# Optimization experiments

Measured on AMD Instinct MI355X. Metric: run time of the kernel, lower is better.

## Reference

```python
import jax, jax.numpy as jnp
import numpy as np

B, H, W, C = 4, 224, 224, 256
HEADS = 8
WIN = 7
N = WIN * WIN  # 49 tokens per window
MLP_HID = 4 * C
EPS = 1e-5


def _rel_index(w):
    coords = np.stack(np.meshgrid(np.arange(w), np.arange(w), indexing='ij'))  # (2,w,w)
    cf = coords.reshape(2, -1)                       # (2, w*w)
    rc = cf[:, :, None] - cf[:, None, :]             # (2, N, N)
    rc = rc.transpose(1, 2, 0).astype(np.int64)      # (N, N, 2)
    rc[:, :, 0] += w - 1
    rc[:, :, 1] += w - 1
    rc[:, :, 0] *= 2 * w - 1
    return jnp.asarray(rc.sum(-1), dtype=jnp.int32)  # (N, N)


def setup_inputs() -> dict:
    key = jax.random.key(0)
    ks = jax.random.split(key, 6)
    std = 0.02
    return {
        'x': jax.random.normal(ks[0], (B, H, W, C), dtype=jnp.float32),
        'norm1_g': jnp.ones((C,), jnp.float32),
        'norm1_b': jnp.zeros((C,), jnp.float32),
        'qkv_w': jax.random.normal(ks[1], (3 * C, C), jnp.float32) * std,
        'qkv_b': jnp.zeros((3 * C,), jnp.float32),
        'bias_table': jax.random.normal(ks[2], ((2 * WIN - 1) ** 2, HEADS), jnp.float32) * std,
        'proj_w': jax.random.normal(ks[3], (C, C), jnp.float32) * std,
        'proj_b': jnp.zeros((C,), jnp.float32),
        'norm2_g': jnp.ones((C,), jnp.float32),
        'norm2_b': jnp.zeros((C,), jnp.float32),
        'fc1_w': jax.random.normal(ks[4], (MLP_HID, C), jnp.float32) * std,
        'fc1_b': jnp.zeros((MLP_HID,), jnp.float32),
        'fc2_w': jax.random.normal(ks[5], (C, MLP_HID), jnp.float32) * std,
        'fc2_b': jnp.zeros((C,), jnp.float32),
        'rel_index': _rel_index(WIN),
    }


def _layernorm(x, g, b):
    mu = jnp.mean(x, axis=-1, keepdims=True)
    var = jnp.mean(jnp.square(x - mu), axis=-1, keepdims=True)
    return (x - mu) * jax.lax.rsqrt(var + EPS) * g + b


def reference(x, norm1_g, norm1_b, qkv_w, qkv_b, bias_table, proj_w, proj_b,
              norm2_g, norm2_b, fc1_w, fc1_b, fc2_w, fc2_b, rel_index):
    Bc, Hc, Wc, Cc = x.shape
    d = Cc // HEADS
    scale = d ** -0.5
    nh, nw = Hc // WIN, Wc // WIN

    shortcut = x
    h = _layernorm(x, norm1_g, norm1_b)

    # window_partition: (B,H,W,C) -> (B*nW, N, C)
    wins = h.reshape(Bc, nh, WIN, nw, WIN, Cc).transpose(0, 1, 3, 2, 4, 5)
    wins = wins.reshape(-1, N, Cc)

    # qkv projection and split into heads
    qkv = wins @ qkv_w.T + qkv_b                                  # (Bw, N, 3C)
    qkv = qkv.reshape(-1, N, 3, HEADS, d).transpose(2, 0, 3, 1, 4)  # (3, Bw, h, N, d)
    q, k, v = qkv[0], qkv[1], qkv[2]

    attn = jnp.einsum('bhnd,bhmd->bhnm', q, k) * scale            # (Bw, h, N, N)
    bias = bias_table[rel_index.reshape(-1)].reshape(N, N, HEADS).transpose(2, 0, 1)
    attn = jax.nn.softmax(attn + bias[None], axis=-1)

    o = jnp.einsum('bhnm,bhmd->bhnd', attn, v)                    # (Bw, h, N, d)
    o = o.transpose(0, 2, 1, 3).reshape(-1, N, Cc)
    o = o @ proj_w.T + proj_b

    # window_reverse: (B*nW, N, C) -> (B,H,W,C)
    o = o.reshape(Bc, nh, nw, WIN, WIN, Cc).transpose(0, 1, 3, 2, 4, 5)
    o = o.reshape(Bc, Hc, Wc, Cc)

    x = shortcut + o
    h2 = _layernorm(x, norm2_g, norm2_b)
    m = jax.nn.gelu(h2 @ fc1_w.T + fc1_b, approximate=False) @ fc2_w.T + fc2_b
    return x + m
```

## Files before the change

kernel.cpp:

```cpp
#include <hip/hip_runtime.h>

typedef unsigned short u16;
typedef __bf16 bf16x8 __attribute__((ext_vector_type(8)));
typedef float f32x4 __attribute__((ext_vector_type(4)));

#define TOKENS 200704
#define QK_ELEMS 51380224UL

__device__ __forceinline__ u16 f2b(float f) {
    __bf16 h = (__bf16)f;
    return __builtin_bit_cast(u16, h);
}

#define GLDS(g, l) __builtin_amdgcn_global_load_lds( \
    (const __attribute__((address_space(1))) void*)(g), \
    (__attribute__((address_space(3))) void*)(l), 16, 0, 0)

#define MFMA __builtin_amdgcn_mfma_f32_16x16x32_bf16

template<int EPI, int WR, int WC>
__global__ __launch_bounds__(512, 4)
void gemm_t(const u16* __restrict__ A, const u16* __restrict__ W,
            const float* __restrict__ bias, int nt, int K,
            u16* __restrict__ outb, float* __restrict__ outf,
            const float* __restrict__ res,
            const float* __restrict__ g2, const float* __restrict__ b2,
            u16* __restrict__ h2o)
{
    constexpr int BM = WR * 64, BN = WC * 64;
    constexpr int ACH = BM / 16;
    constexpr int TCH = (BM + BN) / 16;
    __shared__ u16 As[3][BM * 32];
    __shared__ u16 Bs[3][BN * 32];
    __shared__ float red[EPI == 1 ? 2 * 128 * 4 : 1];

    const int tid  = threadIdx.x;
    const int wave = tid >> 6, lane = tid & 63;

    const int nwg = gridDim.x, bidO = blockIdx.x;
    const int qq = nwg >> 3, rr = nwg & 7;
    const int xcd = bidO & 7, idxx = bidO >> 3;
    const int bid = (xcd < rr) ? (xcd * (qq + 1) + idxx)
                               : (rr * (qq + 1) + (xcd - rr) * qq + idxx);

    const int bm = bid / nt, bn = bid % nt;
    const long m0 = (long)bm * BM;
    const int  n0 = bn * BN;
    const int wr = wave / WC, wc = wave % WC;
    const int lr = lane & 15, lg = lane >> 4;
    const int ccol_s = (((lane & 3) ^ ((lane >> 3) & 3)) * 8);
    const int swzr = (lg ^ ((lr >> 1) & 3)) * 8;

    f32x4 acc[4][4] = {};

    auto stage = [&](int buf, int k0) {
#pragma unroll
        for (int p = 0; p < TCH / 8; ++p) {
            const int q = p * 8 + wave;
            const int rq = (q < ACH) ? q : q - ACH;
            const int row = rq * 16 + (lane >> 2);
            if (q < ACH)
                GLDS(A + (m0 + row) * (long)K + k0 + ccol_s, &As[buf][rq * 512]);
            else
                GLDS(W + (long)(n0 + row) * K + k0 + ccol_s, &Bs[buf][rq * 512]);
        }
    };

    auto compute = [&](int buf) {
        bf16x8 af[4], bfr[4];
#pragma unroll
        for (int fm = 0; fm < 4; ++fm)
            af[fm] = *reinterpret_cast<const bf16x8*>(
                &As[buf][(wr * 64 + fm * 16 + lr) * 32 + swzr]);
#pragma unroll
        for (int fn = 0; fn < 4; ++fn)
            bfr[fn] = *reinterpret_cast<const bf16x8*>(
                &Bs[buf][(wc * 64 + fn * 16 + lr) * 32 + swzr]);
        __builtin_amdgcn_s_setprio(1);
#pragma unroll
        for (int fm = 0; fm < 4; ++fm)
#pragma unroll
            for (int fn = 0; fn < 4; ++fn)
                acc[fm][fn] = MFMA(af[fm], bfr[fn], acc[fm][fn], 0, 0, 0);
        __builtin_amdgcn_s_setprio(0);
    };

    const int nk = K >> 5;
    stage(0, 0);
    stage(1, 32);
    stage(2, 64);
    int k = 96;
    int buf = 0;
    for (int t = 0; t < nk; ++t) {
        if (t + 2 < nk)      asm volatile("s_waitcnt vmcnt(6)" ::: "memory");
        else if (t + 1 < nk) asm volatile("s_waitcnt vmcnt(3)" ::: "memory");
        else                 asm volatile("s_waitcnt vmcnt(0)" ::: "memory");
        __builtin_amdgcn_s_barrier();
        __builtin_amdgcn_sched_barrier(0);
        compute(buf);
        __builtin_amdgcn_s_barrier();
        __builtin_amdgcn_sched_barrier(0);
        if (t + 3 < nk) {
            stage(buf, k); k += 32;
            __builtin_amdgcn_sched_barrier(0);
        }
        buf = (buf == 2) ? 0 : buf + 1;
    }

    if constexpr (EPI == 0 || EPI == 2) {
        u16* st = &As[0][0];
        float bb4[4], sc4[4];
#pragma unroll
        for (int fn = 0; fn < 4; ++fn) {
            const int n = n0 + wc * 64 + fn * 16 + lr;
            bb4[fn] = bias[n];
            sc4[fn] = (EPI == 0 && (n >> 8) == 0) ? 0.17677669529663687f : 1.0f;
        }
        const size_t secbase = (EPI == 0)
            ? (size_t)(n0 >> 8) * QK_ELEMS + (size_t)(n0 & 255) : 0;
#pragma unroll
        for (int h = 0; h < 2; ++h) {
            if ((wr >> 1) == h) {
#pragma unroll
                for (int fm = 0; fm < 4; ++fm) {
#pragma unroll
                    for (int r = 0; r < 4; ++r) {
                        const int lrow = (wr & 1) * 64 + fm * 16 + lg * 4 + r;
                        const int swb = ((lrow >> 2) & 3) << 1;
#pragma unroll
                        for (int fn = 0; fn < 4; ++fn) {
                            const int col = wc * 64 + fn * 16 + lr;
                            const int cs = (col >> 3) ^ swb;
                            float v = acc[fm][fn][r] + bb4[fn];
                            u16 w;
                            if (EPI == 0) {
                                w = f2b(v * sc4[fn]);
                            } else {
                                const float s = v * (1.5957691216f + 0.07135481627f * v * v);
                                w = f2b(v * __builtin_amdgcn_rcpf(1.0f + __expf(-s)));
                            }
                            st[lrow * 128 + cs * 8 + (col & 7)] = w;
                        }
                    }
                }
            }
            asm volatile("s_waitcnt lgkmcnt(0)" ::: "memory");
            __builtin_amdgcn_s_barrier();
#pragma unroll
            for (int it = 0; it < 4; ++it) {
                const int u = it * 512 + tid;
                const int row = u >> 4, chunk = u & 15;
                const int cs = chunk ^ (((row >> 2) & 3) << 1);
                const bf16x8 val = *reinterpret_cast<const bf16x8*>(st + row * 128 + cs * 8);
                const long m = m0 + h * 128 + row;
                if (EPI == 0) {
                    *reinterpret_cast<bf16x8*>(outb + secbase + m * 256 + (chunk << 3)) = val;
                } else {
                    *reinterpret_cast<bf16x8*>(outb + m * 1024 + n0 + (chunk << 3)) = val;
                }
            }
            if (h == 0) {
                asm volatile("s_waitcnt lgkmcnt(0)" ::: "memory");
                __builtin_amdgcn_s_barrier();
            }
        }
    } else if constexpr (EPI == 1) {
        float g2c[4], b2c[4];
#pragma unroll
        for (int fn = 0; fn < 4; ++fn) {
            const int n = wc * 64 + fn * 16 + lr;
            g2c[fn] = g2[n]; b2c[fn] = b2[n];
        }
#pragma unroll
        for (int fm = 0; fm < 4; ++fm) {
#pragma unroll
            for (int r = 0; r < 4; ++r) {
                const long m = m0 + wr * 64 + fm * 16 + lg * 4 + r;
                float s = 0.f, s2 = 0.f;
#pragma unroll
                for (int fn = 0; fn < 4; ++fn) {
                    const int n = wc * 64 + fn * 16 + lr;
                    const float x2 = acc[fm][fn][r] + bias[n] + res[m * 256 + n];
                    acc[fm][fn][r] = x2;
                    outf[m * 256 + n] = x2;
                    s += x2; s2 += x2 * x2;
                }
#pragma unroll
                for (int d = 1; d < 16; d <<= 1) { s += __shfl_xor(s, d); s2 += __shfl_xor(s2, d); }
                if (lr == 0) {
                    const int tok = wr * 64 + fm * 16 + lg * 4 + r;
                    red[(0 * 128 + tok) * 4 + wc] = s;
                    red[(1 * 128 + tok) * 4 + wc] = s2;
                }
            }
        }
        __syncthreads();
#pragma unroll
        for (int fm = 0; fm < 4; ++fm) {
#pragma unroll
            for (int r = 0; r < 4; ++r) {
                const int tok = wr * 64 + fm * 16 + lg * 4 + r;
                const float s = red[(0 * 128 + tok) * 4 + 0] + red[(0 * 128 + tok) * 4 + 1]
                              + red[(0 * 128 + tok) * 4 + 2] + red[(0 * 128 + tok) * 4 + 3];
                const float q = red[(1 * 128 + tok) * 4 + 0] + red[(1 * 128 + tok) * 4 + 1]
                              + red[(1 * 128 + tok) * 4 + 2] + red[(1 * 128 + tok) * 4 + 3];
                const float mu = s * 0.00390625f;
                const float rs = rsqrtf(q * 0.00390625f - mu * mu + 1e-5f);
                const long m = m0 + tok;
#pragma unroll
                for (int fn = 0; fn < 4; ++fn) {
                    const int n = wc * 64 + fn * 16 + lr;
                    h2o[m * 256 + n] = f2b((acc[fm][fn][r] - mu) * rs * g2c[fn] + b2c[fn]);
                }
            }
        }
    } else {
#pragma unroll
        for (int fm = 0; fm < 4; ++fm) {
#pragma unroll
            for (int r = 0; r < 4; ++r) {
                const long m = m0 + wr * 64 + fm * 16 + lg * 4 + r;
#pragma unroll
                for (int fn = 0; fn < 4; ++fn) {
                    const int n = n0 + wc * 64 + fn * 16 + lr;
                    outf[m * 256 + n] += acc[fm][fn][r] + bias[n];
                }
            }
        }
    }
}

__global__ __launch_bounds__(256)
void layernorm_k(const float* __restrict__ in, const float* __restrict__ g,
                 const float* __restrict__ bb, u16* __restrict__ out)
{
    const int token = blockIdx.x * 4 + (threadIdx.x >> 6);
    const int lane = threadIdx.x & 63;
    const float4 v = *reinterpret_cast<const float4*>(in + (size_t)token * 256 + lane * 4);
    float s  = v.x + v.y + v.z + v.w;
    float s2 = v.x * v.x + v.y * v.y + v.z * v.z + v.w * v.w;
#pragma unroll
    for (int m = 1; m < 64; m <<= 1) { s += __shfl_xor(s, m); s2 += __shfl_xor(s2, m); }
    const float mu  = s * (1.0f / 256.0f);
    const float var = s2 * (1.0f / 256.0f) - mu * mu;
    const float rs  = rsqrtf(var + 1e-5f);
    const float4 gv = *reinterpret_cast<const float4*>(g + lane * 4);
    const float4 bv = *reinterpret_cast<const float4*>(bb + lane * 4);
    ushort4 o;
    o.x = f2b((v.x - mu) * rs * gv.x + bv.x);
    o.y = f2b((v.y - mu) * rs * gv.y + bv.y);
    o.z = f2b((v.z - mu) * rs * gv.z + bv.z);
    o.w = f2b((v.w - mu) * rs * gv.w + bv.w);
    const int b = token / 50176, rem = token % 50176;
    const int y = rem / 224, x = rem % 224;
    const int win = (b * 32 + y / 7) * 32 + x / 7;
    const int pos = (y % 7) * 7 + (x % 7);
    const size_t wrow = (size_t)win * 49 + pos;
    *reinterpret_cast<ushort4*>(out + wrow * 256 + lane * 4) = o;
}

__global__ __launch_bounds__(256)
void attn_win(const u16* __restrict__ qkv, const float* __restrict__ biasF,
              u16* __restrict__ outb)
{
    __shared__ u16 plds[4][64 * 72];
    __shared__ u16 vlds[4][2048];
    const int wave = threadIdx.x >> 6, lane = threadIdx.x & 63;
    const int pair = blockIdx.x * 4 + wave;
    const int head = pair & 7, win = pair >> 3;
    const int lr = lane & 15, lg = lane >> 4;

    const u16* Q  = qkv + (size_t)win * 12544 + head * 32;
    const u16* Kp = Q + QK_ELEMS;
    const u16* Vp = Q + 2 * QK_ELEMS;

    bf16x8 qf[4], kf[4];
#pragma unroll
    for (int f = 0; f < 4; ++f) {
        int n = f * 16 + lr; n = n > 48 ? 48 : n;
        qf[f] = *reinterpret_cast<const bf16x8*>(Q  + n * 256 + lg * 8);
        kf[f] = *reinterpret_cast<const bf16x8*>(Kp + n * 256 + lg * 8);
    }

    u16* vl = &vlds[wave][0];
    {
        const int posh = lane >> 1, dsub = (lane & 1) * 8;
#pragma unroll
        for (int db = 0; db < 2; ++db)
#pragma unroll
            for (int half = 0; half < 2; ++half) {
                int pos = half * 32 + posh; if (pos > 48) pos = 48;
                GLDS(Vp + pos * 256 + db * 16 + dsub, vl + db * 1024 + half * 512);
            }
    }

    f32x4 s[4][4] = {};
#pragma unroll
    for (int fm = 0; fm < 4; ++fm)
#pragma unroll
        for (int fn = 0; fn < 4; ++fn)
            s[fm][fn] = MFMA(qf[fm], kf[fn], s[fm][fn], 0, 0, 0);

    const float* bfh = biasF + head * 4096;
    u16* pl = &plds[wave][0];
#pragma unroll
    for (int fm = 0; fm < 4; ++fm) {
        f32x4 bb[4];
#pragma unroll
        for (int fn = 0; fn < 4; ++fn)
            bb[fn] = *reinterpret_cast<const f32x4*>(bfh + ((fm * 4 + fn) << 8) + (lane << 2));
#pragma unroll
        for (int r = 0; r < 4; ++r) {
            const int row = fm * 16 + lg * 4 + r;
            float v0 = s[fm][0][r] + bb[0][r];
            float v1 = s[fm][1][r] + bb[1][r];
            float v2 = s[fm][2][r] + bb[2][r];
            float v3 = s[fm][3][r] + bb[3][r];
            float mx = fmaxf(fmaxf(v0, v1), fmaxf(v2, v3));
#pragma unroll
            for (int d = 1; d < 16; d <<= 1) mx = fmaxf(mx, __shfl_xor(mx, d));
            const float p0 = __expf(v0 - mx), p1 = __expf(v1 - mx);
            const float p2 = __expf(v2 - mx), p3 = __expf(v3 - mx);
            float sum = p0 + p1 + p2 + p3;
#pragma unroll
            for (int d = 1; d < 16; d <<= 1) sum += __shfl_xor(sum, d);
            const float rinv = __builtin_amdgcn_rcpf(sum);
            pl[row * 72 +  0 + lr] = f2b(p0 * rinv);
            pl[row * 72 + 16 + lr] = f2b(p1 * rinv);
            pl[row * 72 + 32 + lr] = f2b(p2 * rinv);
            pl[row * 72 + 48 + lr] = f2b(p3 * rinv);
        }
    }

    asm volatile("s_waitcnt vmcnt(0)" ::: "memory");
    if (lane < 60) {
        const int db = lane / 30, ix = lane % 30;
        f32x4 z = {0.f, 0.f, 0.f, 0.f};
        *reinterpret_cast<f32x4*>(vl + db * 1024 + 784 + ix * 8) = z;
    }
    asm volatile("s_waitcnt lgkmcnt(0)" ::: "memory");
    __builtin_amdgcn_sched_barrier(0);

    const unsigned VB = (unsigned)(unsigned long)
        (__attribute__((address_space(3))) u16*)vl;
    unsigned long long trv[2][2][2];
#pragma unroll
    for (int kc = 0; kc < 2; ++kc)
#pragma unroll
        for (int f2 = 0; f2 < 2; ++f2) {
            const unsigned va = VB + f2 * 2048 + kc * 1024 + lg * 256 + lr * 2;
            asm volatile("ds_read_b64_tr_b16 %0, %1"
                         : "=v"(trv[kc][f2][0]) : "v"(va));
            asm volatile("ds_read_b64_tr_b16 %0, %1 offset:128"
                         : "=v"(trv[kc][f2][1]) : "v"(va));
        }
    asm volatile("s_waitcnt lgkmcnt(0)" ::: "memory");
    __builtin_amdgcn_sched_barrier(0);

    f32x4 o[4][2] = {};
#pragma unroll
    for (int kc = 0; kc < 2; ++kc) {
#pragma unroll
        for (int fm = 0; fm < 4; ++fm) {
            const bf16x8 pa = *reinterpret_cast<const bf16x8*>(
                pl + (fm * 16 + lr) * 72 + kc * 32 + lg * 8);
#pragma unroll
            for (int f2 = 0; f2 < 2; ++f2) {
                union { unsigned long long q[2]; bf16x8 v; } u;
                u.q[0] = trv[kc][f2][0]; u.q[1] = trv[kc][f2][1];
                o[fm][f2] = MFMA(pa, u.v, o[fm][f2], 0, 0, 0);
            }
        }
    }

    const int b = win >> 10, rem = win & 1023, wy = rem >> 5, wx = rem & 31;
#pragma unroll
    for (int fm = 0; fm < 4; ++fm) {
#pragma unroll
        for (int r = 0; r < 4; ++r) {
            const int tok = fm * 16 + lg * 4 + r;
            if (tok > 48) continue;
            const int y = wy * 7 + tok / 7, xx = wx * 7 + tok % 7;
            const size_t mrow = ((size_t)(b * 224 + y)) * 224 + xx;
#pragma unroll
            for (int f2 = 0; f2 < 2; ++f2)
                outb[mrow * 256 + head * 32 + f2 * 16 + lr] = f2b(o[fm][f2][r]);
        }
    }
}

__global__ __launch_bounds__(256)
void cvt_w(const float* __restrict__ qw, const float* __restrict__ pw,
           const float* __restrict__ f1, const float* __restrict__ f2,
           u16* __restrict__ outw)
{
    const int t = blockIdx.x * 256 + threadIdx.x;
    float v;
    if (t < 196608) v = qw[t];
    else if (t < 262144) v = pw[t - 196608];
    else if (t < 524288) v = f1[t - 262144];
    else v = f2[t - 524288];
    outw[t] = f2b(v);
}

__global__ __launch_bounds__(256)
void bias_pre(const float* __restrict__ btab, const int* __restrict__ relidx,
              float* __restrict__ biasF)
{
    const int t = blockIdx.x * 256 + threadIdx.x;
    const int head = t >> 10, rem = t & 1023;
    const int fr = rem >> 6, lane = rem & 63;
    const int fm = fr >> 2, fn = fr & 3;
    const int lr = lane & 15, lg = lane >> 4;
    const int col = fn * 16 + lr;
    f32x4 o;
#pragma unroll
    for (int r = 0; r < 4; ++r) {
        int row = fm * 16 + lg * 4 + r; if (row > 48) row = 48;
        o[r] = (col > 48) ? -1e30f : btab[relidx[row * 49 + col] * 8 + head];
    }
    *reinterpret_cast<f32x4*>(biasF + t * 4) = o;
}

extern "C" void kernel_launch(void* const* d_in, const int* in_sizes, int n_in,
                              void* d_out, int out_size, void* d_ws, size_t ws_size,
                              hipStream_t stream)
{
    const float* x      = (const float*)d_in[0];
    const float* n1g    = (const float*)d_in[1];
    const float* n1b    = (const float*)d_in[2];
    const float* qkv_w  = (const float*)d_in[3];
    const float* qkv_b  = (const float*)d_in[4];
    const float* btab   = (const float*)d_in[5];
    const float* proj_w = (const float*)d_in[6];
    const float* proj_b = (const float*)d_in[7];
    const float* n2g    = (const float*)d_in[8];
    const float* n2b    = (const float*)d_in[9];
    const float* fc1_w  = (const float*)d_in[10];
    const float* fc1_b  = (const float*)d_in[11];
    const float* fc2_w  = (const float*)d_in[12];
    const float* fc2_b  = (const float*)d_in[13];
    const int*   relidx = (const int*)d_in[14];
    float* out = (float*)d_out;

    char* ws = (char*)d_ws;
    u16*   wbf   = (u16*)ws;
    float* biasF = (float*)(ws + 1572864);
    u16*   hbuf  = (u16*)(ws + 1703936);
    u16*   rbuf  = (u16*)(ws + 1703936 + 102760448);
    const size_t r_avail = ws_size - (1703936 + 102760448);

    const u16* Wq  = wbf;
    const u16* Wp  = wbf + 196608;
    const u16* Wf1 = wbf + 262144;
    const u16* Wf2 = wbf + 524288;

    cvt_w<<<3072, 256, 0, stream>>>(qkv_w, proj_w, fc1_w, fc2_w, wbf);
    bias_pre<<<32, 256, 0, stream>>>(btab, relidx, biasF);
    layernorm_k<<<50176, 256, 0, stream>>>(x, n1g, n1b, hbuf);

    gemm_t<0, 4, 2><<<784 * 6, 512, 0, stream>>>(hbuf, Wq, qkv_b, 6, 256,
                                                 rbuf, nullptr, nullptr, nullptr, nullptr, nullptr);
    attn_win<<<8192, 256, 0, stream>>>(rbuf, biasF, hbuf);

    gemm_t<1, 2, 4><<<1568, 512, 0, stream>>>(hbuf, Wp, proj_b, 1, 256,
                                              nullptr, out, x, n2g, n2b, hbuf);

    long rows_per = 100352;
    if ((long)(r_avail / 2048) < rows_per) rows_per = 50176;
    for (long r0 = 0; r0 < TOKENS; r0 += rows_per) {
        const long rows = (TOKENS - r0 < rows_per) ? (TOKENS - r0) : rows_per;
        gemm_t<2, 4, 2><<<(int)((rows / 256) * 8), 512, 0, stream>>>(
            hbuf + r0 * 256, Wf1, fc1_b, 8, 256, rbuf, nullptr, nullptr, nullptr, nullptr, nullptr);
        gemm_t<3, 4, 2><<<(int)((rows / 256) * 2), 512, 0, stream>>>(
            rbuf, Wf2, fc2_b, 2, 1024, nullptr, out + r0 * 256, nullptr, nullptr, nullptr, nullptr);
    }
}
```

Before: 988.8 us.

## Keep activations in window order and scatter to image layout in epilogues

The attention kernel now writes its output contiguously in window-token order instead of scattering to image rows. The proj and fc2 epilogues map each window-ordered row back to its image token to index the residual and output, so hbuf and the MLP intermediates stay in window order. The weight-convert and bias-precompute kernels are merged into one launch, and the MLP chunk size is halved, which likely keeps the intermediate buffer more cache-resident at the cost of more launches. The residual reads and output writes in the epilogues become strided by window position.

Measured after the change: 994.1 us, median of 2. No clear change (+0.5%).

```diff
diff --git a/kernel.cpp b/kernel.cpp
--- a/kernel.cpp
+++ b/kernel.cpp
@@ -12,6 +12,13 @@
     return __builtin_bit_cast(u16, h);
 }
 
+__device__ __forceinline__ int win2tok(int gm) {
+    const int win = gm / 49, pos = gm - win * 49;
+    const int b = win >> 10, wrem = win & 1023, wy = wrem >> 5, wx = wrem & 31;
+    const int y = wy * 7 + pos / 7, x = wx * 7 + pos % 7;
+    return b * 50176 + y * 224 + x;
+}
+
 #define GLDS(g, l) __builtin_amdgcn_global_load_lds( \
     (const __attribute__((address_space(1))) void*)(g), \
     (__attribute__((address_space(3))) void*)(l), 16, 0, 0)
@@ -21,7 +28,7 @@
 template<int EPI, int WR, int WC>
 __global__ __launch_bounds__(512, 4)
 void gemm_t(const u16* __restrict__ A, const u16* __restrict__ W,
-            const float* __restrict__ bias, int nt, int K,
+            const float* __restrict__ bias, int nt, int K, long moff,
             u16* __restrict__ outb, float* __restrict__ outf,
             const float* __restrict__ res,
             const float* __restrict__ g2, const float* __restrict__ b2,
@@ -176,13 +183,14 @@
 #pragma unroll
             for (int r = 0; r < 4; ++r) {
                 const long m = m0 + wr * 64 + fm * 16 + lg * 4 + r;
+                const size_t trow = (size_t)win2tok((int)m) * 256;
                 float s = 0.f, s2 = 0.f;
 #pragma unroll
                 for (int fn = 0; fn < 4; ++fn) {
                     const int n = wc * 64 + fn * 16 + lr;
-                    const float x2 = acc[fm][fn][r] + bias[n] + res[m * 256 + n];
+                    const float x2 = acc[fm][fn][r] + bias[n] + res[trow + n];
                     acc[fm][fn][r] = x2;
-                    outf[m * 256 + n] = x2;
+                    outf[trow + n] = x2;
                     s += x2; s2 += x2 * x2;
                 }
 #pragma unroll
@@ -220,10 +228,11 @@
 #pragma unroll
             for (int r = 0; r < 4; ++r) {
                 const long m = m0 + wr * 64 + fm * 16 + lg * 4 + r;
+                const size_t trow = (size_t)win2tok((int)(m + moff)) * 256;
 #pragma unroll
                 for (int fn = 0; fn < 4; ++fn) {
                     const int n = n0 + wc * 64 + fn * 16 + lr;
-                    outf[m * 256 + n] += acc[fm][fn][r] + bias[n];
+                    outf[trow + n] += acc[fm][fn][r] + bias[n];
                 }
             }
         }
@@ -373,53 +382,50 @@
         }
     }
 
-    const int b = win >> 10, rem = win & 1023, wy = rem >> 5, wx = rem & 31;
+    u16* ob = outb + (size_t)win * 12544 + head * 32;
 #pragma unroll
     for (int fm = 0; fm < 4; ++fm) {
 #pragma unroll
         for (int r = 0; r < 4; ++r) {
             const int tok = fm * 16 + lg * 4 + r;
             if (tok > 48) continue;
-            const int y = wy * 7 + tok / 7, xx = wx * 7 + tok % 7;
-            const size_t mrow = ((size_t)(b * 224 + y)) * 224 + xx;
 #pragma unroll
             for (int f2 = 0; f2 < 2; ++f2)
-                outb[mrow * 256 + head * 32 + f2 * 16 + lr] = f2b(o[fm][f2][r]);
+                ob[tok * 256 + f2 * 16 + lr] = f2b(o[fm][f2][r]);
         }
     }
 }
 
 __global__ __launch_bounds__(256)
-void cvt_w(const float* __restrict__ qw, const float* __restrict__ pw,
-           const float* __restrict__ f1, const float* __restrict__ f2,
-           u16* __restrict__ outw)
+void prep(const float* __restrict__ qw, const float* __restrict__ pw,
+          const float* __restrict__ f1, const float* __restrict__ f2,
+          u16* __restrict__ outw,
+          const float* __restrict__ btab, const int* __restrict__ relidx,
+          float* __restrict__ biasF)
 {
-    const int t = blockIdx.x * 256 + threadIdx.x;
-    float v;
-    if (t < 196608) v = qw[t];
-    else if (t < 262144) v = pw[t - 196608];
-    else if (t < 524288) v = f1[t - 262144];
-    else v = f2[t - 524288];
-    outw[t] = f2b(v);
-}
-
-__global__ __launch_bounds__(256)
-void bias_pre(const float* __restrict__ btab, const int* __restrict__ relidx,
-              float* __restrict__ biasF)
-{
-    const int t = blockIdx.x * 256 + threadIdx.x;
-    const int head = t >> 10, rem = t & 1023;
-    const int fr = rem >> 6, lane = rem & 63;
-    const int fm = fr >> 2, fn = fr & 3;
-    const int lr = lane & 15, lg = lane >> 4;
-    const int col = fn * 16 + lr;
-    f32x4 o;
-#pragma unroll
-    for (int r = 0; r < 4; ++r) {
-        int row = fm * 16 + lg * 4 + r; if (row > 48) row = 48;
-        o[r] = (col > 48) ? -1e30f : btab[relidx[row * 49 + col] * 8 + head];
-    }
-    *reinterpret_cast<f32x4*>(biasF + t * 4) = o;
+    if (blockIdx.x < 3072) {
+        const int t = blockIdx.x * 256 + threadIdx.x;
+        float v;
+        if (t < 196608) v = qw[t];
+        else if (t < 262144) v = pw[t - 196608];
+        else if (t < 524288) v = f1[t - 262144];
+        else v = f2[t - 524288];
+        outw[t] = f2b(v);
+    } else {
+        const int t = (blockIdx.x - 3072) * 256 + threadIdx.x;
+        const int head = t >> 10, rem = t & 1023;
+        const int fr = rem >> 6, lane = rem & 63;
+        const int fm = fr >> 2, fn = fr & 3;
+        const int lr = lane & 15, lg = lane >> 4;
+        const int col = fn * 16 + lr;
+        f32x4 o;
+#pragma unroll
+        for (int r = 0; r < 4; ++r) {
+            int row = fm * 16 + lg * 4 + r; if (row > 48) row = 48;
+            o[r] = (col > 48) ? -1e30f : btab[relidx[row * 49 + col] * 8 + head];
+        }
+        *reinterpret_cast<f32x4*>(biasF + t * 4) = o;
+    }
 }
 
 extern "C" void kernel_launch(void* const* d_in, const int* in_sizes, int n_in,
@@ -455,24 +461,24 @@
     const u16* Wf1 = wbf + 262144;
     const u16* Wf2 = wbf + 524288;
 
-    cvt_w<<<3072, 256, 0, stream>>>(qkv_w, proj_w, fc1_w, fc2_w, wbf);
-    bias_pre<<<32, 256, 0, stream>>>(btab, relidx, biasF);
+    prep<<<3104, 256, 0, stream>>>(qkv_w, proj_w, fc1_w, fc2_w, wbf,
+                                   btab, relidx, biasF);
     layernorm_k<<<50176, 256, 0, stream>>>(x, n1g, n1b, hbuf);
 
-    gemm_t<0, 4, 2><<<784 * 6, 512, 0, stream>>>(hbuf, Wq, qkv_b, 6, 256,
+    gemm_t<0, 4, 2><<<784 * 6, 512, 0, stream>>>(hbuf, Wq, qkv_b, 6, 256, 0,
                                                  rbuf, nullptr, nullptr, nullptr, nullptr, nullptr);
     attn_win<<<8192, 256, 0, stream>>>(rbuf, biasF, hbuf);
 
-    gemm_t<1, 2, 4><<<1568, 512, 0, stream>>>(hbuf, Wp, proj_b, 1, 256,
+    gemm_t<1, 2, 4><<<1568, 512, 0, stream>>>(hbuf, Wp, proj_b, 1, 256, 0,
                                               nullptr, out, x, n2g, n2b, hbuf);
 
-    long rows_per = 100352;
-    if ((long)(r_avail / 2048) < rows_per) rows_per = 50176;
+    long rows_per = 50176;
+    if ((long)(r_avail / 2048) < rows_per) rows_per = 25088;
     for (long r0 = 0; r0 < TOKENS; r0 += rows_per) {
         const long rows = (TOKENS - r0 < rows_per) ? (TOKENS - r0) : rows_per;
         gemm_t<2, 4, 2><<<(int)((rows / 256) * 8), 512, 0, stream>>>(
-            hbuf + r0 * 256, Wf1, fc1_b, 8, 256, rbuf, nullptr, nullptr, nullptr, nullptr, nullptr);
+            hbuf + r0 * 256, Wf1, fc1_b, 8, 256, 0, rbuf, nullptr, nullptr, nullptr, nullptr, nullptr);
         gemm_t<3, 4, 2><<<(int)((rows / 256) * 2), 512, 0, stream>>>(
-            rbuf, Wf2, fc2_b, 2, 1024, nullptr, out + r0 * 256, nullptr, nullptr, nullptr, nullptr);
-    }
-}
+            rbuf, Wf2, fc2_b, 2, 1024, r0, nullptr, out, nullptr, nullptr, nullptr, nullptr);
+    }
+}
```
